# Performance work log

Hardware: AMD Instinct MI355X
Metric: run time of the kernel (lower is better)

## Reference

```python
import jax, jax.numpy as jnp
import numpy as np

S = 768        # SPATIAL_SIZE
M = 16         # URESNET_FILTERS
NUM_CLASS = 5
N = 2_000_000  # active voxels
BN_EPS = 1e-4  # sparseconvnet BatchNormReLU default eps


def setup_inputs() -> dict:
    rng = np.random.default_rng(0)
    # unique voxel linear indices in [0, S^3) -> unique (x,y,z) active sites
    raw = rng.integers(0, S ** 3, size=3_000_000, dtype=np.int64)
    uniq = rng.permutation(np.unique(raw))[:N]
    x = uniq // (S * S)
    y = (uniq // S) % S
    z = uniq % S
    pc = np.zeros((N, 5), dtype=np.float32)
    pc[:, 0], pc[:, 1], pc[:, 2] = x, y, z
    pc[:, 3] = 0.0   # batch id column (sliced away by the forward)
    pc[:, 4] = 1.0   # feature value; also used as 4th coord (batch) by the code
    key = jax.random.key(0)
    k1, k2, k3, k4, k5 = jax.random.split(key, 5)
    W = jax.random.normal(k1, (27, M), jnp.float32) * 0.2          # 3^3 offsets, 1->M channels
    gamma = jax.random.uniform(k2, (M,), jnp.float32, 0.5, 1.5)
    beta = jax.random.normal(k3, (M,), jnp.float32) * 0.1
    lin_w = jax.random.normal(k4, (M, NUM_CLASS), jnp.float32) / np.sqrt(M)
    lin_b = jax.random.normal(k5, (NUM_CLASS,), jnp.float32) * 0.1
    return {"point_cloud": jnp.asarray(pc), "W": W, "gamma": gamma,
            "beta": beta, "lin_w": lin_w, "lin_b": lin_b}


def reference(point_cloud, W, gamma, beta, lin_w, lin_b):
    n = point_cloud.shape[0]
    # coords = cat(xyz, last column) exactly as the torch forward does
    coords = jnp.concatenate([point_cloud[:, :-2], point_cloud[:, -1:]], axis=1)
    feats = point_cloud[:, -1]                      # (N,) single input feature
    ci = coords.astype(jnp.int32)                   # values fit in int32 (< 2^31)
    xx, yy, zz, bb = ci[:, 0], ci[:, 1], ci[:, 2], ci[:, 3]
    keys = ((bb * S + xx) * S + yy) * S + zz        # unique linear key per site
    order = jnp.argsort(keys)
    skeys = keys[order]
    sfeats = feats[order]
    out = jnp.zeros((n, M), dtype=point_cloud.dtype)
    # submanifold 3x3x3 conv: for each kernel offset, gather neighbor feature
    # where a matching active site exists, rank-1 update with W[k]
    k = 0
    for dx in (-1, 0, 1):
        for dy in (-1, 0, 1):
            for dz in (-1, 0, 1):
                nx, ny, nz = xx + dx, yy + dy, zz + dz
                inb = (nx >= 0) & (nx < S) & (ny >= 0) & (ny < S) & (nz >= 0) & (nz < S)
                nkey = keys + ((dx * S + dy) * S + dz)
                pos = jnp.clip(jnp.searchsorted(skeys, nkey), 0, n - 1)
                hit = inb & (skeys[pos] == nkey)
                f = jnp.where(hit, sfeats[pos], 0.0)   # (N,)
                out = out + f[:, None] * W[k][None, :]
                k += 1
    # BatchNormReLU over active sites (training-mode batch stats)
    mean = out.mean(axis=0)
    var = out.var(axis=0)
    h = jax.nn.relu((out - mean) * jax.lax.rsqrt(var + BN_EPS) * gamma + beta)
    return h @ lin_w + lin_b                         # (N, NUM_CLASS)
```

## Files before the change

kernel.cpp:

```cpp
#include <hip/hip_runtime.h>
#include <stdint.h>

#define SS 768
#define CH 16
#define NCLS 5
#define BN_EPS 1e-4f
#define NBX 48
#define NB  (NBX * NBX)
#define G   512
#define TW  18
#define ZW  25
#define CBS 257
#define RCAP 1280
#define SEG 36

typedef float vf4 __attribute__((ext_vector_type(4)));

__global__ void __launch_bounds__(512) count_k(const float* __restrict__ pc,
                                               uint32_t* __restrict__ cnt,
                                               uint32_t* __restrict__ recs0,
                                               uint32_t* __restrict__ flag, int n) {
    __shared__ uint32_t h[NB];
    int t = threadIdx.x, g = blockIdx.x;
    if (g == 0 && t == 0) *flag = 0;
    for (int j = t; j < NB; j += 512) h[j] = 0;
    __syncthreads();
    int chunk = (n + G - 1) / G;
    int lo = g * chunk, hi = min(n, lo + chunk);
    for (int i = lo + t; i < hi; i += 512) {
        float4 v = *(const float4*)(pc + (size_t)i * 5);
        int x = (int)v.x;
        int y = (int)v.y;
        int z = (int)v.z;
        atomicAdd(&h[(x >> 4) * NBX + (y >> 4)], 1u);
        recs0[i] = ((uint32_t)x << 20) | ((uint32_t)y << 10) | (uint32_t)z;
    }
    __syncthreads();
    for (int j = t; j < NB; j += 512) cnt[(size_t)g * NB + j] = h[j];
}

__global__ void __launch_bounds__(64) scan1_k(uint32_t* __restrict__ cnt,
                                              uint32_t* __restrict__ tot,
                                              uint32_t* __restrict__ base,
                                              uint32_t* __restrict__ flag) {
    int b = blockIdx.x * 64 + threadIdx.x;
    uint32_t carry = 0;
    for (int g = 0; g < G; g += 32) {
        uint32_t v[32];
#pragma unroll
        for (int k = 0; k < 32; k++) v[k] = cnt[(size_t)(g + k) * NB + b];
#pragma unroll
        for (int k = 0; k < 32; k++) {
            uint32_t x = v[k];
            cnt[(size_t)(g + k) * NB + b] = carry;
            carry += x;
        }
    }
    tot[b] = carry;
    __threadfence();
    __shared__ uint32_t rank;
    if (threadIdx.x == 0) rank = atomicAdd(flag, 1u);
    __syncthreads();
    if (rank != gridDim.x - 1) return;

    int lane = threadIdx.x;
    uint32_t v[SEG];
#pragma unroll
    for (int k = 0; k < SEG; k++) v[k] = tot[lane * SEG + k];
    uint32_t e[SEG];
    uint32_t run = 0;
#pragma unroll
    for (int k = 0; k < SEG; k++) { e[k] = run; run += v[k]; }
    uint32_t s = run;
    for (int off = 1; off < 64; off <<= 1) {
        uint32_t u = __shfl_up(s, off, 64);
        if (lane >= off) s += u;
    }
    uint32_t laneOff = s - run;
#pragma unroll
    for (int k = 0; k < SEG; k++) base[lane * SEG + k] = laneOff + e[k];
    if (lane == 63) base[NB] = laneOff + run;
}

__global__ void __launch_bounds__(512) scatter2_k(
        const uint32_t* __restrict__ recs0, const uint32_t* __restrict__ cnt,
        const uint32_t* __restrict__ base, unsigned long long* __restrict__ recsA, int n) {
    __shared__ uint32_t pos[NB];
    int t = threadIdx.x, g = blockIdx.x;
    for (int j = t; j < NB; j += 512) pos[j] = base[j] + cnt[(size_t)g * NB + j];
    __syncthreads();
    int chunk = (n + G - 1) / G;
    int lo = g * chunk, hi = min(n, lo + chunk);
    for (int i = lo + t; i < hi; i += 512) {
        uint32_t key = recs0[i];
        int x = key >> 20, y = (key >> 10) & 1023;
        int b = (x >> 4) * NBX + (y >> 4);
        uint32_t p = atomicAdd(&pos[b], 1u);
        recsA[p] = ((unsigned long long)key << 21) | (uint32_t)i;
    }
}

__global__ void sortcells_k(const unsigned long long* __restrict__ recsA,
                            const uint32_t* __restrict__ base,
                            unsigned long long* __restrict__ recs2,
                            uint32_t* __restrict__ cellbase) {
    __shared__ unsigned long long lrec[RCAP];
    __shared__ uint32_t h[256], pos2[256], wt[4], wo[4];
    int t = threadIdx.x, b = blockIdx.x;
    uint32_t s0 = base[b], s1 = base[b + 1];
    int cb = (int)(s1 - s0);
    bool fits = cb <= RCAP;
    if (fits) for (int r = t; r < cb; r += 256) lrec[r] = recsA[s0 + r];
    h[t] = 0;
    __syncthreads();
    for (int r = t; r < cb; r += 256) {
        unsigned long long rec = fits ? lrec[r] : recsA[s0 + r];
        int x = (int)(rec >> 41) & 1023, y = (int)(rec >> 31) & 1023;
        atomicAdd(&h[(x & 15) * 16 + (y & 15)], 1u);
    }
    __syncthreads();
    int lane = t & 63, wid = t >> 6;
    uint32_t v = h[t], s = v;
    for (int off = 1; off < 64; off <<= 1) {
        uint32_t u = __shfl_up(s, off, 64);
        if (lane >= off) s += u;
    }
    if (lane == 63) wt[wid] = s;
    __syncthreads();
    if (t == 0) { uint32_t c = 0; for (int w = 0; w < 4; w++) { uint32_t x = wt[w]; wo[w] = c; c += x; } }
    __syncthreads();
    uint32_t excl = s - v + wo[wid];
    cellbase[(size_t)b * CBS + t] = excl;
    if (t == 255) cellbase[(size_t)b * CBS + 256] = excl + v;
    pos2[t] = excl;
    __syncthreads();
    for (int r = t; r < cb; r += 256) {
        unsigned long long rec = fits ? lrec[r] : recsA[s0 + r];
        int x = (int)(rec >> 41) & 1023, y = (int)(rec >> 31) & 1023;
        uint32_t p = atomicAdd(&pos2[(x & 15) * 16 + (y & 15)], 1u);
        recs2[s0 + p] = rec;
    }
}

__global__ void __launch_bounds__(256) tile_k(
        const unsigned long long* __restrict__ recs2,
        const uint32_t* __restrict__ base, const uint32_t* __restrict__ cellbase,
        const float* __restrict__ W, uint32_t* __restrict__ masks,
        float* __restrict__ partials) {
    __shared__ uint32_t lbm[TW * TW * ZW];
    __shared__ float sW[27 * CH];
    __shared__ float sred[4][32];
    __shared__ uint32_t sbeg[40], slen[40], soff[41];
    int t = threadIdx.x;
    int b = blockIdx.x;
    int tx = b / NBX, ty = b % NBX;
    int x0 = tx * 16 - 1, y0 = ty * 16 - 1;

    unsigned long long* lb8 = (unsigned long long*)lbm;
    for (int j = t; j < TW * TW * ZW / 2; j += 256) lb8[j] = 0ull;
    for (int j = t; j < 27 * CH; j += 256) sW[j] = W[j];

    if (t < 39) {
        int nb = -1, c0 = 0, c1 = 0;
        if (t == 0)      { nb = b; c0 = 0; c1 = 256; }
        else if (t == 1) { if (tx + 1 < NBX) nb = (tx + 1) * NBX + ty; c0 = 0;   c1 = 16;  }
        else if (t == 2) { if (tx > 0)       nb = (tx - 1) * NBX + ty; c0 = 240; c1 = 256; }
        else if (t < 19) { int lx = t - 3;  if (ty > 0)       nb = tx * NBX + (ty - 1); c0 = lx * 16 + 15; c1 = c0 + 1; }
        else if (t < 35) { int lx = t - 19; if (ty + 1 < NBX) nb = tx * NBX + (ty + 1); c0 = lx * 16;      c1 = c0 + 1; }
        else if (t == 35) { if (tx + 1 < NBX && ty > 0)       nb = (tx + 1) * NBX + (ty - 1); c0 = 15;  c1 = 16;  }
        else if (t == 36) { if (tx + 1 < NBX && ty + 1 < NBX) nb = (tx + 1) * NBX + (ty + 1); c0 = 0;   c1 = 1;   }
        else if (t == 37) { if (tx > 0 && ty > 0)             nb = (tx - 1) * NBX + (ty - 1); c0 = 255; c1 = 256; }
        else              { if (tx > 0 && ty + 1 < NBX)       nb = (tx - 1) * NBX + (ty + 1); c0 = 240; c1 = 241; }
        uint32_t g0 = 0, len = 0;
        if (nb >= 0) {
            uint32_t bb = base[nb];
            uint32_t cb0 = cellbase[(size_t)nb * CBS + c0];
            uint32_t cb1 = cellbase[(size_t)nb * CBS + c1];
            g0 = bb + cb0; len = cb1 - cb0;
        }
        sbeg[t] = g0; slen[t] = len;
    }
    __syncthreads();
    if (t < 64) {
        uint32_t len = (t < 39) ? slen[t] : 0;
        uint32_t s = len;
        for (int off = 1; off < 64; off <<= 1) {
            uint32_t u = __shfl_up(s, off, 64);
            if (t >= off) s += u;
        }
        if (t < 40) soff[t] = s - len;
    }
    __syncthreads();
    uint32_t T = soff[39];
    for (uint32_t w = t; w < T; w += 256) {
        int lo = 0, hi = 38;
        while (lo < hi) { int mid = (lo + hi + 1) >> 1; if (soff[mid] <= w) lo = mid; else hi = mid - 1; }
        uint32_t gr = sbeg[lo] + (w - soff[lo]);
        unsigned long long rec = recs2[gr];
        int x = (int)(rec >> 41) & 1023;
        int y = (int)(rec >> 31) & 1023;
        int z = (int)(rec >> 21) & 1023;
        int p = z + 1;
        atomicOr(&lbm[((x - x0) * TW + (y - y0)) * ZW + (p >> 5)], 1u << (p & 31));
    }
    __syncthreads();

    float acc1[CH], acc2[CH];
#pragma unroll
    for (int m = 0; m < CH; m++) { acc1[m] = 0.f; acc2[m] = 0.f; }

    uint32_t s0 = base[b], s1 = base[b + 1];
    for (uint32_t i = s0 + t; i < s1; i += 256) {
        unsigned long long rec = recs2[i];
        int x = (int)(rec >> 41) & 1023;
        int y = (int)(rec >> 31) & 1023;
        int z = (int)(rec >> 21) & 1023;
        uint32_t idx = (uint32_t)(rec & 0x1FFFFFu);
        int bc = ((x - x0) * TW + (y - y0)) * ZW + (z >> 5);
        uint32_t sh = (uint32_t)z & 31;
        uint32_t mask = 0;
#pragma unroll
        for (int dx = -1; dx <= 1; dx++) {
#pragma unroll
            for (int dy = -1; dy <= 1; dy++) {
                int c = bc + (dx * TW + dy) * ZW;
                uint64_t dw = (uint64_t)lbm[c] | ((uint64_t)lbm[c + 1] << 32);
                mask |= ((uint32_t)(dw >> sh) & 7u) << (((dx + 1) * 3 + (dy + 1)) * 3);
            }
        }
        masks[idx] = mask;

        float o[CH];
#pragma unroll
        for (int m = 0; m < CH; m++) o[m] = 0.f;
        uint32_t mm = mask;
        while (mm) {
            int k = __builtin_ctz(mm);
            mm &= mm - 1;
#pragma unroll
            for (int m = 0; m < CH; m++) o[m] += sW[k * CH + m];
        }
#pragma unroll
        for (int m = 0; m < CH; m++) { acc1[m] += o[m]; acc2[m] += o[m] * o[m]; }
    }

    int lane = t & 63, wid = t >> 6;
#pragma unroll
    for (int m = 0; m < CH; m++) {
        float v = acc1[m];
        float v2 = acc2[m];
        for (int off = 32; off; off >>= 1) {
            v += __shfl_xor(v, off, 64);
            v2 += __shfl_xor(v2, off, 64);
        }
        if (lane == 0) { sred[wid][m] = v; sred[wid][16 + m] = v2; }
    }
    __syncthreads();
    if (t < 32) {
        float s = 0.f;
        for (int w = 0; w < 4; w++) s += sred[w][t];
        partials[(size_t)t * NB + b] = s;
    }
}

__global__ void reduce_k(const float* __restrict__ partials, float* __restrict__ sums) {
    __shared__ float sd[256];
    int t = threadIdx.x, s = blockIdx.x;
    float acc = 0.f;
    for (int i = t; i < NB; i += 256) acc += partials[(size_t)s * NB + i];
    sd[t] = acc;
    __syncthreads();
    for (int h = 128; h; h >>= 1) {
        if (t < h) sd[t] += sd[t + h];
        __syncthreads();
    }
    if (t == 0) sums[s] = sd[0];
}

__global__ void __launch_bounds__(256) final3_k(
        const uint32_t* __restrict__ masks, const float* __restrict__ W,
        const float* __restrict__ sums, const float* __restrict__ gamma,
        const float* __restrict__ beta, const float* __restrict__ lin_w,
        const float* __restrict__ lin_b, float* __restrict__ out, int n) {
    __shared__ float sW[27 * CH];
    __shared__ float sA[CH], sB[CH], sLW[CH * NCLS], sLB[NCLS];
    __shared__ float so[256 * NCLS];
    int t = threadIdx.x;
    for (int j = t; j < 27 * CH; j += 256) sW[j] = W[j];
    if (t < CH) {
        float mean = sums[t] / (float)n;
        float var = sums[16 + t] / (float)n - mean * mean;
        float istd = rsqrtf(var + BN_EPS);
        float a = istd * gamma[t];
        sA[t] = a;
        sB[t] = beta[t] - mean * a;
    }
    if (t < CH * NCLS) sLW[t] = lin_w[t];
    if (t < NCLS) sLB[t] = lin_b[t];
    __syncthreads();

    int i = blockIdx.x * 256 + t;
    float res[NCLS];
#pragma unroll
    for (int c = 0; c < NCLS; c++) res[c] = sLB[c];
    if (i < n) {
        uint32_t mm = masks[i];
        float o[CH];
#pragma unroll
        for (int m = 0; m < CH; m++) o[m] = 0.f;
        while (mm) {
            int k = __builtin_ctz(mm);
            mm &= mm - 1;
#pragma unroll
            for (int m = 0; m < CH; m++) o[m] += sW[k * CH + m];
        }
#pragma unroll
        for (int m = 0; m < CH; m++) {
            float h = fmaxf(o[m] * sA[m] + sB[m], 0.f);
#pragma unroll
            for (int c = 0; c < NCLS; c++) res[c] += h * sLW[m * NCLS + c];
        }
    }
#pragma unroll
    for (int c = 0; c < NCLS; c++) so[t * NCLS + c] = res[c];
    __syncthreads();

    size_t ob = (size_t)blockIdx.x * 256 * NCLS;
    int npts = n - blockIdx.x * 256;
    if (npts >= 256) {
        for (int j = t; j < 256 * NCLS / 4; j += 256) {
            vf4 v = *(const vf4*)&so[j * 4];
            __builtin_nontemporal_store(v, (vf4*)(out + ob + (size_t)j * 4));
        }
    } else if (npts > 0) {
        for (int j = t; j < npts * NCLS; j += 256) out[ob + j] = so[j];
    }
}

extern "C" void kernel_launch(void* const* d_in, const int* in_sizes, int n_in,
                              void* d_out, int out_size, void* d_ws, size_t ws_size,
                              hipStream_t stream) {
    const float* pc    = (const float*)d_in[0];
    const float* W     = (const float*)d_in[1];
    const float* gamma = (const float*)d_in[2];
    const float* beta  = (const float*)d_in[3];
    const float* lin_w = (const float*)d_in[4];
    const float* lin_b = (const float*)d_in[5];
    float* out = (float*)d_out;

    int n = in_sizes[0] / 5;
    int nblk = (n + 255) / 256;

    char* ws = (char*)d_ws;
    float* sums = (float*)ws;
    uint32_t* flag = (uint32_t*)(ws + 128);
    uint32_t* cnt = (uint32_t*)(ws + 256);
    size_t off = 256 + (size_t)G * NB * 4;
    uint32_t* tot = (uint32_t*)(ws + off);   off += (size_t)NB * 4;
    uint32_t* base = (uint32_t*)(ws + off);  off += (size_t)(NB + 1) * 4;
    off = (off + 255) & ~(size_t)255;
    uint32_t* recs0 = (uint32_t*)(ws + off);                     off += (size_t)n * 4;
    off = (off + 255) & ~(size_t)255;
    unsigned long long* recsA = (unsigned long long*)(ws + off); off += (size_t)n * 8;
    unsigned long long* recs2 = (unsigned long long*)(ws + off); off += (size_t)n * 8;
    uint32_t* cellbase = (uint32_t*)(ws + off); off += (size_t)NB * CBS * 4;
    off = (off + 255) & ~(size_t)255;
    uint32_t* masks = (uint32_t*)(ws + off); off += (size_t)n * 4;
    float* partials = (float*)(ws + off);    off += (size_t)NB * 32 * 4;
    if (ws_size < off) return;

    count_k    <<<G, 512, 0, stream>>>(pc, cnt, recs0, flag, n);
    scan1_k    <<<NB / 64, 64, 0, stream>>>(cnt, tot, base, flag);
    scatter2_k <<<G, 512, 0, stream>>>(recs0, cnt, base, recsA, n);
    sortcells_k<<<NB, 256, 0, stream>>>(recsA, base, recs2, cellbase);
    tile_k     <<<NB, 256, 0, stream>>>(recs2, base, cellbase, W, masks, partials);
    reduce_k   <<<32, 256, 0, stream>>>(partials, sums);
    final3_k   <<<nblk, 256, 0, stream>>>(masks, W, sums, gamma, beta, lin_w, lin_b, out, n);
}
```

Measured before the change: 228.9 us.

## Split tile bitmap into two z-halves to halve LDS footprint

```diff
diff --git a/kernel.cpp b/kernel.cpp
--- a/kernel.cpp
+++ b/kernel.cpp
@@ -9,7 +9,8 @@
 #define NB  (NBX * NBX)
 #define G   512
 #define TW  18
-#define ZW  25
+#define ZS  384
+#define ZWP 13
 #define CBS 257
 #define RCAP 1280
 #define SEG 36
@@ -147,7 +148,7 @@
         const uint32_t* __restrict__ base, const uint32_t* __restrict__ cellbase,
         const float* __restrict__ W, uint32_t* __restrict__ masks,
         float* __restrict__ partials) {
-    __shared__ uint32_t lbm[TW * TW * ZW];
+    __shared__ uint32_t lbm[TW * TW * ZWP + 2];
     __shared__ float sW[27 * CH];
     __shared__ float sred[4][32];
     __shared__ uint32_t sbeg[40], slen[40], soff[41];
@@ -156,8 +157,6 @@
     int tx = b / NBX, ty = b % NBX;
     int x0 = tx * 16 - 1, y0 = ty * 16 - 1;
 
-    unsigned long long* lb8 = (unsigned long long*)lbm;
-    for (int j = t; j < TW * TW * ZW / 2; j += 256) lb8[j] = 0ull;
     for (int j = t; j < 27 * CH; j += 256) sW[j] = W[j];
 
     if (t < 39) {
@@ -191,57 +190,79 @@
         if (t < 40) soff[t] = s - len;
     }
     __syncthreads();
+
+    float acc1[CH], acc2[CH];
+#pragma unroll
+    for (int m = 0; m < CH; m++) { acc1[m] = 0.f; acc2[m] = 0.f; }
+
+    uint32_t s0 = base[b], s1 = base[b + 1];
     uint32_t T = soff[39];
-    for (uint32_t w = t; w < T; w += 256) {
-        int lo = 0, hi = 38;
-        while (lo < hi) { int mid = (lo + hi + 1) >> 1; if (soff[mid] <= w) lo = mid; else hi = mid - 1; }
-        uint32_t gr = sbeg[lo] + (w - soff[lo]);
-        unsigned long long rec = recs2[gr];
-        int x = (int)(rec >> 41) & 1023;
-        int y = (int)(rec >> 31) & 1023;
-        int z = (int)(rec >> 21) & 1023;
-        int p = z + 1;
-        atomicOr(&lbm[((x - x0) * TW + (y - y0)) * ZW + (p >> 5)], 1u << (p & 31));
-    }
-    __syncthreads();
-
-    float acc1[CH], acc2[CH];
-#pragma unroll
-    for (int m = 0; m < CH; m++) { acc1[m] = 0.f; acc2[m] = 0.f; }
-
-    uint32_t s0 = base[b], s1 = base[b + 1];
-    for (uint32_t i = s0 + t; i < s1; i += 256) {
-        unsigned long long rec = recs2[i];
-        int x = (int)(rec >> 41) & 1023;
-        int y = (int)(rec >> 31) & 1023;
-        int z = (int)(rec >> 21) & 1023;
-        uint32_t idx = (uint32_t)(rec & 0x1FFFFFu);
-        int bc = ((x - x0) * TW + (y - y0)) * ZW + (z >> 5);
-        uint32_t sh = (uint32_t)z & 31;
-        uint32_t mask = 0;
-#pragma unroll
-        for (int dx = -1; dx <= 1; dx++) {
-#pragma unroll
-            for (int dy = -1; dy <= 1; dy++) {
-                int c = bc + (dx * TW + dy) * ZW;
-                uint64_t dw = (uint64_t)lbm[c] | ((uint64_t)lbm[c + 1] << 32);
-                mask |= ((uint32_t)(dw >> sh) & 7u) << (((dx + 1) * 3 + (dy + 1)) * 3);
+    unsigned long long* lb8 = (unsigned long long*)lbm;
+
+    for (int phase = 0; phase < 2; phase++) {
+        int z0 = phase * ZS;
+        for (int j = t; j < (TW * TW * ZWP + 2) / 2; j += 256) lb8[j] = 0ull;
+        __syncthreads();
+
+        for (uint32_t i = s0 + t; i < s1; i += 256) {
+            unsigned long long rec = recs2[i];
+            int x = (int)(rec >> 41) & 1023;
+            int y = (int)(rec >> 31) & 1023;
+            int z = (int)(rec >> 21) & 1023;
+            int p = z - z0 + 1;
+            if ((unsigned)p <= (unsigned)(ZS + 1))
+                atomicOr(&lbm[((x - x0) * TW + (y - y0)) * ZWP + (p >> 5)], 1u << (p & 31));
+        }
+        for (uint32_t w = t; w < T; w += 256) {
+            int lo = 0, hi = 38;
+            while (lo < hi) { int mid = (lo + hi + 1) >> 1; if (soff[mid] <= w) lo = mid; else hi = mid - 1; }
+            uint32_t gr = sbeg[lo] + (w - soff[lo]);
+            unsigned long long rec = recs2[gr];
+            int x = (int)(rec >> 41) & 1023;
+            int y = (int)(rec >> 31) & 1023;
+            int z = (int)(rec >> 21) & 1023;
+            int p = z - z0 + 1;
+            if ((unsigned)p <= (unsigned)(ZS + 1))
+                atomicOr(&lbm[((x - x0) * TW + (y - y0)) * ZWP + (p >> 5)], 1u << (p & 31));
+        }
+        __syncthreads();
+
+        for (uint32_t i = s0 + t; i < s1; i += 256) {
+            unsigned long long rec = recs2[i];
+            int z = (int)(rec >> 21) & 1023;
+            int pp = z - z0;
+            if ((unsigned)pp >= (unsigned)ZS) continue;
+            int x = (int)(rec >> 41) & 1023;
+            int y = (int)(rec >> 31) & 1023;
+            uint32_t idx = (uint32_t)(rec & 0x1FFFFFu);
+            int bc = ((x - x0) * TW + (y - y0)) * ZWP + (pp >> 5);
+            uint32_t sh = (uint32_t)pp & 31;
+            uint32_t mask = 0;
+#pragma unroll
+            for (int dx = -1; dx <= 1; dx++) {
+#pragma unroll
+                for (int dy = -1; dy <= 1; dy++) {
+                    int c = bc + (dx * TW + dy) * ZWP;
+                    uint64_t dw = (uint64_t)lbm[c] | ((uint64_t)lbm[c + 1] << 32);
+                    mask |= ((uint32_t)(dw >> sh) & 7u) << (((dx + 1) * 3 + (dy + 1)) * 3);
+                }
             }
-        }
-        masks[idx] = mask;
-
-        float o[CH];
-#pragma unroll
-        for (int m = 0; m < CH; m++) o[m] = 0.f;
-        uint32_t mm = mask;
-        while (mm) {
-            int k = __builtin_ctz(mm);
-            mm &= mm - 1;
-#pragma unroll
-            for (int m = 0; m < CH; m++) o[m] += sW[k * CH + m];
-        }
-#pragma unroll
-        for (int m = 0; m < CH; m++) { acc1[m] += o[m]; acc2[m] += o[m] * o[m]; }
+            masks[idx] = mask;
+
+            float o[CH];
+#pragma unroll
+            for (int m = 0; m < CH; m++) o[m] = 0.f;
+            uint32_t mm = mask;
+            while (mm) {
+                int k = __builtin_ctz(mm);
+                mm &= mm - 1;
+#pragma unroll
+                for (int m = 0; m < CH; m++) o[m] += sW[k * CH + m];
+            }
+#pragma unroll
+            for (int m = 0; m < CH; m++) { acc1[m] += o[m]; acc2[m] += o[m] * o[m]; }
+        }
+        __syncthreads();
     }
 
     int lane = t & 63, wid = t >> 6;
```

Measured after the change: 238.5 us. 4.2% more time.
